# Optimization experiments

Hardware: AMD Instinct MI355X
Metric: run time of the kernel (lower is better)

Reference implementation:

```python
import jax, jax.numpy as jnp
import numpy as np

DIM = 1024
NUM_HEADS = 16
HEAD_DIM = DIM // NUM_HEADS
MLP_HIDDEN = 4 * DIM
SCALE = HEAD_DIM ** -0.5
EPS = 1e-5


def setup_inputs() -> dict:
    key = jax.random.key(0)
    ks = jax.random.split(key, 6)
    s = (2.0 / DIM) ** 0.5
    sd = (2.0 / MLP_HIDDEN) ** 0.5
    return {
        "x": jax.random.normal(ks[0], (2, 2048, DIM), dtype=jnp.float32),
        "attn_qkv_weight": jax.random.normal(ks[1], (3 * DIM, DIM), dtype=jnp.float32) * s,
        "attn_out_weight": jax.random.normal(ks[2], (DIM, DIM), dtype=jnp.float32) * s,
        "norm1_weight": jnp.ones((DIM,), jnp.float32),
        "norm1_bias": jnp.zeros((DIM,), jnp.float32),
        "mlp_gate_weight": jax.random.normal(ks[3], (MLP_HIDDEN, DIM), dtype=jnp.float32) * s,
        "mlp_up_weight": jax.random.normal(ks[4], (MLP_HIDDEN, DIM), dtype=jnp.float32) * s,
        "mlp_down_weight": jax.random.normal(ks[5], (DIM, MLP_HIDDEN), dtype=jnp.float32) * sd,
        "norm2_weight": jnp.ones((DIM,), jnp.float32),
        "norm2_bias": jnp.zeros((DIM,), jnp.float32),
    }


def _layer_norm(x, w, b):
    mean = x.mean(axis=-1, keepdims=True)
    var = jnp.mean(jnp.square(x - mean), axis=-1, keepdims=True)
    return (x - mean) / jnp.sqrt(var + EPS) * w + b


def reference(x, attn_qkv_weight, attn_out_weight, norm1_weight, norm1_bias,
              mlp_gate_weight, mlp_up_weight, mlp_down_weight, norm2_weight, norm2_bias):
    B, S, D = x.shape
    residual1 = x
    xn = _layer_norm(x, norm1_weight, norm1_bias)
    qkv = xn @ attn_qkv_weight.T                      # [B,S,3D]
    qkv = qkv.reshape(B, S, 3, NUM_HEADS, HEAD_DIM).transpose(2, 0, 3, 1, 4)
    q, k, v = qkv[0], qkv[1], qkv[2]                  # [B,H,S,hd]
    scores = jnp.einsum('bhqd,bhkd->bhqk', q, k) * SCALE  # full O(S^2) matrix
    attn = jax.nn.softmax(scores, axis=-1)            # no causal mask (default False)
    out = jnp.einsum('bhqk,bhkd->bhqd', attn, v)      # [B,H,S,hd]
    out = out.transpose(0, 2, 1, 3).reshape(B, S, D)
    x2 = residual1 + out @ attn_out_weight.T
    xn2 = _layer_norm(x2, norm2_weight, norm2_bias)
    gate = xn2 @ mlp_gate_weight.T
    up = xn2 @ mlp_up_weight.T
    hidden = jax.nn.silu(gate) * up
    return x2 + hidden @ mlp_down_weight.T
```

## Files before the change

### kernel.cpp

```cpp
#include <hip/hip_runtime.h>

typedef float f32x4 __attribute__((ext_vector_type(4)));
typedef __bf16 bf16x8 __attribute__((ext_vector_type(8)));
typedef unsigned int u32;

#define DEV __device__ __forceinline__

DEV void gload_lds16(const void* g, void* l) {
  __builtin_amdgcn_global_load_lds(
      (const __attribute__((address_space(1))) u32*)g,
      (__attribute__((address_space(3))) u32*)l, 16, 0, 0);
}

DEV int xcd_swz(int flat, int nwg) {
  return (flat & 7) * (nwg >> 3) + (flat >> 3);
}

__global__ __launch_bounds__(256) void cvt_bf16(const float* __restrict__ in,
                                                __bf16* __restrict__ o, int n) {
  int i = (blockIdx.x * 256 + threadIdx.x) * 8;
  if (i >= n) return;
  float4 a = *(const float4*)(in + i);
  float4 b = *(const float4*)(in + i + 4);
  union { bf16x8 v; __bf16 e[8]; } u;
  u.e[0] = (__bf16)a.x; u.e[1] = (__bf16)a.y; u.e[2] = (__bf16)a.z; u.e[3] = (__bf16)a.w;
  u.e[4] = (__bf16)b.x; u.e[5] = (__bf16)b.y; u.e[6] = (__bf16)b.z; u.e[7] = (__bf16)b.w;
  *(bf16x8*)(o + i) = u.v;
}

__global__ __launch_bounds__(256) void ln_kernel(const float* __restrict__ x,
                                                 const float* __restrict__ w,
                                                 const float* __restrict__ b,
                                                 __bf16* __restrict__ o) {
  const int row = blockIdx.x, tid = threadIdx.x;
  const float4 v = ((const float4*)(x + (size_t)row * 1024))[tid];
  float s  = v.x + v.y + v.z + v.w;
  float s2 = v.x * v.x + v.y * v.y + v.z * v.z + v.w * v.w;
  for (int off = 32; off; off >>= 1) {
    s  += __shfl_down(s, off);
    s2 += __shfl_down(s2, off);
  }
  __shared__ float rs[4], rs2[4];
  if ((tid & 63) == 0) { rs[tid >> 6] = s; rs2[tid >> 6] = s2; }
  __syncthreads();
  float S = rs[0] + rs[1] + rs[2] + rs[3];
  float S2 = rs2[0] + rs2[1] + rs2[2] + rs2[3];
  float mean = S * (1.0f / 1024.0f);
  float var = S2 * (1.0f / 1024.0f) - mean * mean;
  float inv = rsqrtf(var + 1e-5f);
  const float4 wv = ((const float4*)w)[tid];
  const float4 bv = ((const float4*)b)[tid];
  union { ushort4 u4; __bf16 e[4]; } u;
  u.e[0] = (__bf16)((v.x - mean) * inv * wv.x + bv.x);
  u.e[1] = (__bf16)((v.y - mean) * inv * wv.y + bv.y);
  u.e[2] = (__bf16)((v.z - mean) * inv * wv.z + bv.z);
  u.e[3] = (__bf16)((v.w - mean) * inv * wv.w + bv.w);
  *(ushort4*)(o + (size_t)row * 1024 + tid * 4) = u.u4;
}

template <int EPI, int MI>
__global__ __launch_bounds__(256) void gemm_bt(const __bf16* __restrict__ A,
                                               const __bf16* __restrict__ B,
                                               void* __restrict__ Cout,
                                               const float* __restrict__ Res,
                                               int M, int N, int K) {
  constexpr int BM = MI * 32;
  __shared__ __align__(16) __bf16 As[2][BM * 32];
  __shared__ __align__(16) __bf16 Bs[2][128 * 32];
  const int tid = threadIdx.x;
  const int lane = tid & 63;
  const int w = tid >> 6;
  const int wr = w >> 1, wc = w & 1;
  const int l15 = lane & 15, g = lane >> 4;

  const int nbx = gridDim.x;
  const int logical = xcd_swz(blockIdx.y * nbx + blockIdx.x, nbx * gridDim.y);
  const int bm = (logical / nbx) * BM, bn = (logical % nbx) * 128;

  f32x4 acc[MI][4] = {};

  auto stage = [&](int buf, int k0) {
#pragma unroll
    for (int p = 0; p < MI / 2; ++p) {
      const int ch = p * 256 + tid;
      const int row = ch >> 2, c = ch & 3;
      gload_lds16(A + (size_t)(bm + row) * K + k0 + c * 8, &As[buf][(p * 256 + w * 64) * 8]);
    }
#pragma unroll
    for (int p = 0; p < 2; ++p) {
      const int ch = p * 256 + tid;
      const int row = ch >> 2, c = ch & 3;
      gload_lds16(B + (size_t)(bn + row) * K + k0 + c * 8, &Bs[buf][(p * 256 + w * 64) * 8]);
    }
  };

  stage(0, 0);
  asm volatile("s_waitcnt vmcnt(0)" ::: "memory");
  __syncthreads();

  int cur = 0;
  for (int k0 = 0;;) {
    const int nk = k0 + 32;
    if (nk < K) stage(cur ^ 1, nk);
    bf16x8 af[MI], bfr[4];
#pragma unroll
    for (int i = 0; i < MI; ++i)
      af[i] = *(const bf16x8*)(&As[cur][(wr * (MI * 16) + i * 16 + l15) * 32 + g * 8]);
#pragma unroll
    for (int j = 0; j < 4; ++j)
      bfr[j] = *(const bf16x8*)(&Bs[cur][(wc * 64 + j * 16 + l15) * 32 + g * 8]);
#pragma unroll
    for (int i = 0; i < MI; ++i)
#pragma unroll
      for (int j = 0; j < 4; ++j)
        acc[i][j] = __builtin_amdgcn_mfma_f32_16x16x32_bf16(af[i], bfr[j], acc[i][j], 0, 0, 0);
    if (nk >= K) break;
    asm volatile("s_waitcnt vmcnt(0)" ::: "memory");
    __syncthreads();
    cur ^= 1;
    k0 = nk;
  }

  const int r0 = bm + wr * (MI * 16) + g * 4;
  const int c0 = bn + wc * 64 + l15;
#pragma unroll
  for (int i = 0; i < MI; ++i)
#pragma unroll
    for (int j = 0; j < 4; ++j)
#pragma unroll
      for (int r = 0; r < 4; ++r) {
        const size_t idx = (size_t)(r0 + i * 16 + r) * N + (c0 + j * 16);
        const float v = acc[i][j][r];
        if (EPI == 0) ((__bf16*)Cout)[idx] = (__bf16)v;
        else          ((float*)Cout)[idx] = v + Res[idx];
      }
}

__global__ __launch_bounds__(256, 2) void gemm_mlp(const __bf16* __restrict__ A,
                                                   const __bf16* __restrict__ BG,
                                                   const __bf16* __restrict__ BU,
                                                   __bf16* __restrict__ H,
                                                   int M, int N, int K) {
  __shared__ __align__(16) __bf16 As[2][128 * 32];
  __shared__ __align__(16) __bf16 Bg[2][128 * 32];
  __shared__ __align__(16) __bf16 Bu[2][128 * 32];
  const int tid = threadIdx.x;
  const int lane = tid & 63;
  const int w = tid >> 6;
  const int wr = w >> 1, wc = w & 1;
  const int l15 = lane & 15, g = lane >> 4;

  const int nbx = gridDim.x;
  const int logical = xcd_swz(blockIdx.y * nbx + blockIdx.x, nbx * gridDim.y);
  const int bm = (logical / nbx) * 128, bn = (logical % nbx) * 128;

  f32x4 accg[4][4] = {};
  f32x4 accu[4][4] = {};

  auto stage = [&](int buf, int k0) {
#pragma unroll
    for (int p = 0; p < 2; ++p) {
      const int ch = p * 256 + tid;
      const int row = ch >> 2, c = ch & 3;
      const int dst = (p * 256 + w * 64) * 8;
      gload_lds16(A + (size_t)(bm + row) * K + k0 + c * 8, &As[buf][dst]);
      gload_lds16(BG + (size_t)(bn + row) * K + k0 + c * 8, &Bg[buf][dst]);
      gload_lds16(BU + (size_t)(bn + row) * K + k0 + c * 8, &Bu[buf][dst]);
    }
  };

  stage(0, 0);
  asm volatile("s_waitcnt vmcnt(0)" ::: "memory");
  __syncthreads();

  int cur = 0;
  for (int k0 = 0;;) {
    const int nk = k0 + 32;
    if (nk < K) stage(cur ^ 1, nk);
    bf16x8 af[4], bgf[4], buf_[4];
#pragma unroll
    for (int i = 0; i < 4; ++i)
      af[i] = *(const bf16x8*)(&As[cur][(wr * 64 + i * 16 + l15) * 32 + g * 8]);
#pragma unroll
    for (int j = 0; j < 4; ++j) {
      bgf[j] = *(const bf16x8*)(&Bg[cur][(wc * 64 + j * 16 + l15) * 32 + g * 8]);
      buf_[j] = *(const bf16x8*)(&Bu[cur][(wc * 64 + j * 16 + l15) * 32 + g * 8]);
    }
#pragma unroll
    for (int i = 0; i < 4; ++i)
#pragma unroll
      for (int j = 0; j < 4; ++j) {
        accg[i][j] = __builtin_amdgcn_mfma_f32_16x16x32_bf16(af[i], bgf[j], accg[i][j], 0, 0, 0);
        accu[i][j] = __builtin_amdgcn_mfma_f32_16x16x32_bf16(af[i], buf_[j], accu[i][j], 0, 0, 0);
      }
    if (nk >= K) break;
    asm volatile("s_waitcnt vmcnt(0)" ::: "memory");
    __syncthreads();
    cur ^= 1;
    k0 = nk;
  }

  const int r0 = bm + wr * 64 + g * 4;
  const int c0 = bn + wc * 64 + l15;
#pragma unroll
  for (int i = 0; i < 4; ++i)
#pragma unroll
    for (int j = 0; j < 4; ++j)
#pragma unroll
      for (int r = 0; r < 4; ++r) {
        const float gt = accg[i][j][r];
        const float ut = accu[i][j][r];
        const float h = gt / (1.0f + __expf(-gt)) * ut;
        H[(size_t)(r0 + i * 16 + r) * N + (c0 + j * 16)] = (__bf16)h;
      }
}

__global__ __launch_bounds__(256) void transpose_v(const __bf16* __restrict__ qkv,
                                                   __bf16* __restrict__ vT) {
  const int st = blockIdx.x, bh = blockIdx.y;
  const int b = bh >> 4, h = bh & 15;
  __shared__ __bf16 tile[64][80];
  const int tid = threadIdx.x;
#pragma unroll
  for (int it = 0; it < 2; ++it) {
    const int idx = it * 256 + tid;
    const int r = idx >> 3, c0 = (idx & 7) * 8;
    bf16x8 v = *(const bf16x8*)(qkv + (size_t)(b * 2048 + st * 64 + r) * 3072 + 2048 + h * 64 + c0);
    *(bf16x8*)&tile[r][c0] = v;
  }
  __syncthreads();
#pragma unroll
  for (int it = 0; it < 2; ++it) {
    const int idx = it * 256 + tid;
    const int d = idx >> 3, s0 = (idx & 7) * 8;
    union { bf16x8 v; __bf16 e[8]; } u;
#pragma unroll
    for (int j = 0; j < 8; ++j) u.e[j] = tile[s0 + j][d];
    *(bf16x8*)(vT + (size_t)(bh * 64 + d) * 2048 + st * 64 + s0) = u.v;
  }
}

__global__ __launch_bounds__(256) void attn_kernel(const __bf16* __restrict__ qkv,
                                                   const __bf16* __restrict__ vT,
                                                   __bf16* __restrict__ outp) {
  const int logical = xcd_swz(blockIdx.y * 32 + blockIdx.x, 1024);
  const int qt = logical & 31, bh = logical >> 5;
  const int b = bh >> 4, h = bh & 15;
  const int tid = threadIdx.x, lane = tid & 63, w = tid >> 6;
  const int l15 = lane & 15, g = lane >> 4;
  const float CSC = 0.125f * 1.44269504f;

  __shared__ __align__(16) __bf16 Ks[64 * 64];
  __shared__ __align__(16) __bf16 Vs[64 * 64];
  __shared__ __align__(16) __bf16 Ps[4][16 * 80];

  const int qrow = qt * 64 + w * 16 + l15;
  const size_t qbase = (size_t)(b * 2048 + qrow) * 3072 + h * 64;
  const bf16x8 qf0 = *(const bf16x8*)(qkv + qbase + g * 8);
  const bf16x8 qf1 = *(const bf16x8*)(qkv + qbase + 32 + g * 8);

  f32x4 o_acc[4] = {};
  float l_r[4] = {0.f, 0.f, 0.f, 0.f};

  const size_t kgbase = (size_t)(b * 2048) * 3072 + 1024 + h * 64;
  const size_t vgbase = (size_t)bh * 64 * 2048;

  for (int t = 0; t < 32; ++t) {
    const int kv0 = t * 64;
#pragma unroll
    for (int p = 0; p < 2; ++p) {
      const int ch = p * 256 + w * 64 + lane;
      const int row = ch >> 3, c = ch & 7;
      const int gc = c ^ (row & 7);
      gload_lds16(qkv + kgbase + (size_t)(kv0 + row) * 3072 + gc * 8, Ks + (p * 256 + w * 64) * 8);
      gload_lds16(vT + vgbase + (size_t)row * 2048 + kv0 + gc * 8, Vs + (p * 256 + w * 64) * 8);
    }
    asm volatile("s_waitcnt vmcnt(0)" ::: "memory");
    __syncthreads();

    f32x4 sf[4];
    __builtin_amdgcn_s_setprio(1);
#pragma unroll
    for (int ni = 0; ni < 4; ++ni) {
      const int krow = ni * 16 + l15;
      const __bf16* kb = Ks + krow * 64;
      const bf16x8 kf0 = *(const bf16x8*)(kb + ((g ^ (krow & 7)) * 8));
      const bf16x8 kf1 = *(const bf16x8*)(kb + (((4 + g) ^ (krow & 7)) * 8));
      f32x4 z = {0.f, 0.f, 0.f, 0.f};
      z = __builtin_amdgcn_mfma_f32_16x16x32_bf16(qf0, kf0, z, 0, 0, 0);
      z = __builtin_amdgcn_mfma_f32_16x16x32_bf16(qf1, kf1, z, 0, 0, 0);
      sf[ni] = z;
    }
    __builtin_amdgcn_s_setprio(0);

#pragma unroll
    for (int ni = 0; ni < 4; ++ni)
#pragma unroll
      for (int r = 0; r < 4; ++r) {
        const float pv = exp2f(sf[ni][r] * CSC);
        sf[ni][r] = pv;
        l_r[r] += pv;
      }

    __bf16* pw = Ps[w];
#pragma unroll
    for (int ni = 0; ni < 4; ++ni)
#pragma unroll
      for (int r = 0; r < 4; ++r) {
        const int row = g * 4 + r;
        const int pc = (ni * 2 + (l15 >> 3)) ^ (row & 7);
        pw[row * 80 + pc * 8 + (l15 & 7)] = (__bf16)sf[ni][r];
      }
    asm volatile("" ::: "memory");
    const bf16x8 pa0 = *(const bf16x8*)(pw + l15 * 80 + ((g ^ (l15 & 7)) * 8));
    const bf16x8 pa1 = *(const bf16x8*)(pw + l15 * 80 + (((4 + g) ^ (l15 & 7)) * 8));

    __builtin_amdgcn_s_setprio(1);
#pragma unroll
    for (int ni = 0; ni < 4; ++ni) {
      const int vrow = ni * 16 + l15;
      const __bf16* vb = Vs + vrow * 64;
      const bf16x8 vf0 = *(const bf16x8*)(vb + ((g ^ (vrow & 7)) * 8));
      const bf16x8 vf1 = *(const bf16x8*)(vb + (((4 + g) ^ (vrow & 7)) * 8));
      o_acc[ni] = __builtin_amdgcn_mfma_f32_16x16x32_bf16(pa0, vf0, o_acc[ni], 0, 0, 0);
      o_acc[ni] = __builtin_amdgcn_mfma_f32_16x16x32_bf16(pa1, vf1, o_acc[ni], 0, 0, 0);
    }
    __builtin_amdgcn_s_setprio(0);
    __syncthreads();
  }

#pragma unroll
  for (int mk = 1; mk < 16; mk <<= 1)
#pragma unroll
    for (int r = 0; r < 4; ++r) l_r[r] += __shfl_xor(l_r[r], mk);
#pragma unroll
  for (int r = 0; r < 4; ++r) {
    const int orow = qt * 64 + w * 16 + g * 4 + r;
    const float invl = 1.0f / l_r[r];
#pragma unroll
    for (int ni = 0; ni < 4; ++ni)
      outp[(size_t)(b * 2048 + orow) * 1024 + h * 64 + ni * 16 + l15] =
          (__bf16)(o_acc[ni][r] * invl);
  }
}

extern "C" void kernel_launch(void* const* d_in, const int* in_sizes, int n_in,
                              void* d_out, int out_size, void* d_ws, size_t ws_size,
                              hipStream_t stream) {
  const float* x     = (const float*)d_in[0];
  const float* Wqkv  = (const float*)d_in[1];
  const float* Wout  = (const float*)d_in[2];
  const float* n1w   = (const float*)d_in[3];
  const float* n1b   = (const float*)d_in[4];
  const float* Wgate = (const float*)d_in[5];
  const float* Wup   = (const float*)d_in[6];
  const float* Wdown = (const float*)d_in[7];
  const float* n2w   = (const float*)d_in[8];
  const float* n2b   = (const float*)d_in[9];
  float* out = (float*)d_out;
  char* ws = (char*)d_ws;
  const size_t MB = 1u << 20;

  __bf16* XN  = (__bf16*)(ws + 0);
  __bf16* QKV = (__bf16*)(ws + 8 * MB);
  __bf16* VT  = (__bf16*)(ws + 32 * MB);
  __bf16* ATT = (__bf16*)(ws + 40 * MB);
  float*  X2  = (float*)(ws + 48 * MB);
  __bf16* H   = QKV;
  __bf16* WQ  = (__bf16*)(ws + 64 * MB);
  __bf16* WO  = (__bf16*)(ws + 70 * MB);
  __bf16* WG  = (__bf16*)(ws + 72 * MB);
  __bf16* WU  = (__bf16*)(ws + 80 * MB);
  __bf16* WD  = (__bf16*)(ws + 88 * MB);

  cvt_bf16<<<3145728 / 2048, 256, 0, stream>>>(Wqkv, WQ, 3145728);
  cvt_bf16<<<1048576 / 2048, 256, 0, stream>>>(Wout, WO, 1048576);
  cvt_bf16<<<4194304 / 2048, 256, 0, stream>>>(Wgate, WG, 4194304);
  cvt_bf16<<<4194304 / 2048, 256, 0, stream>>>(Wup, WU, 4194304);
  cvt_bf16<<<4194304 / 2048, 256, 0, stream>>>(Wdown, WD, 4194304);

  ln_kernel<<<4096, 256, 0, stream>>>(x, n1w, n1b, XN);
  gemm_bt<0, 4><<<dim3(24, 32), 256, 0, stream>>>(XN, WQ, QKV, nullptr, 4096, 3072, 1024);
  transpose_v<<<dim3(32, 32), 256, 0, stream>>>(QKV, VT);
  attn_kernel<<<dim3(32, 32), 256, 0, stream>>>(QKV, VT, ATT);
  gemm_bt<1, 2><<<dim3(8, 64), 256, 0, stream>>>(ATT, WO, X2, x, 4096, 1024, 1024);
  ln_kernel<<<4096, 256, 0, stream>>>(X2, n2w, n2b, XN);
  gemm_mlp<<<dim3(32, 32), 256, 0, stream>>>(XN, WG, WU, H, 4096, 4096, 1024);
  gemm_bt<1, 2><<<dim3(8, 64), 256, 0, stream>>>(H, WD, out, X2, 4096, 1024, 4096);

  (void)in_sizes; (void)n_in; (void)out_size; (void)ws_size;
}
```

Before: 355.3 us.

## Deepen GEMM prefetch with partial vmcnt waits, fragment-ordered LDS, grouped tile swizzle

Restructures the GEMM main loops so two K-tiles are in flight, waiting with partial vmcnt counts instead of draining all loads before each step. The LDS staging layout is reordered so each 16-row MFMA fragment sits contiguously, which lets each lane read with a simple lane*8 offset and avoids bank conflicts. Tile indices are also regrouped in bands of 8 row-tiles to improve L2 reuse. This adds an extra barrier per iteration and relies on hand-computed vmcnt values matching the number of loads issued per stage.

```diff
diff --git a/kernel.cpp b/kernel.cpp
--- a/kernel.cpp
+++ b/kernel.cpp
@@ -5,6 +5,7 @@
 typedef unsigned int u32;
 
 #define DEV __device__ __forceinline__
+#define WAITVM(n) asm volatile("s_waitcnt vmcnt(" #n ")" ::: "memory")
 
 DEV void gload_lds16(const void* g, void* l) {
   __builtin_amdgcn_global_load_lds(
@@ -58,6 +59,7 @@
   *(ushort4*)(o + (size_t)row * 1024 + tid * 4) = u.u4;
 }
 
+
 template <int EPI, int MI>
 __global__ __launch_bounds__(256) void gemm_bt(const __bf16* __restrict__ A,
                                                const __bf16* __restrict__ B,
@@ -65,6 +67,7 @@
                                                const float* __restrict__ Res,
                                                int M, int N, int K) {
   constexpr int BM = MI * 32;
+  constexpr int L = MI / 2 + 2;
   __shared__ __align__(16) __bf16 As[2][BM * 32];
   __shared__ __align__(16) __bf16 Bs[2][128 * 32];
   const int tid = threadIdx.x;
@@ -75,7 +78,9 @@
 
   const int nbx = gridDim.x;
   const int logical = xcd_swz(blockIdx.y * nbx + blockIdx.x, nbx * gridDim.y);
-  const int bm = (logical / nbx) * BM, bn = (logical % nbx) * 128;
+  const int per = 8 * nbx, grp = logical / per, rem = logical % per;
+  const int bm = (grp * 8 + (rem & 7)) * BM;
+  const int bn = (rem >> 3) * 128;
 
   f32x4 acc[MI][4] = {};
 
@@ -83,42 +88,45 @@
 #pragma unroll
     for (int p = 0; p < MI / 2; ++p) {
       const int ch = p * 256 + tid;
-      const int row = ch >> 2, c = ch & 3;
-      gload_lds16(A + (size_t)(bm + row) * K + k0 + c * 8, &As[buf][(p * 256 + w * 64) * 8]);
+      const int S = ch >> 6, u = ch & 63;
+      gload_lds16(A + (size_t)(bm + S * 16 + (u & 15)) * K + k0 + (u >> 4) * 8,
+                  &As[buf][(p * 256 + w * 64) * 8]);
     }
 #pragma unroll
     for (int p = 0; p < 2; ++p) {
       const int ch = p * 256 + tid;
-      const int row = ch >> 2, c = ch & 3;
-      gload_lds16(B + (size_t)(bn + row) * K + k0 + c * 8, &Bs[buf][(p * 256 + w * 64) * 8]);
+      const int S = ch >> 6, u = ch & 63;
+      gload_lds16(B + (size_t)(bn + S * 16 + (u & 15)) * K + k0 + (u >> 4) * 8,
+                  &Bs[buf][(p * 256 + w * 64) * 8]);
     }
   };
 
+  const int NT = K >> 5;
   stage(0, 0);
-  asm volatile("s_waitcnt vmcnt(0)" ::: "memory");
-  __syncthreads();
-
-  int cur = 0;
-  for (int k0 = 0;;) {
-    const int nk = k0 + 32;
-    if (nk < K) stage(cur ^ 1, nk);
+  stage(1, 32);
+
+  for (int t = 0; t < NT; ++t) {
+    if (t + 1 < NT) {
+      if (L == 3) WAITVM(3); else WAITVM(4);
+    } else {
+      WAITVM(0);
+    }
+    __syncthreads();
+    const int cur = t & 1;
     bf16x8 af[MI], bfr[4];
 #pragma unroll
     for (int i = 0; i < MI; ++i)
-      af[i] = *(const bf16x8*)(&As[cur][(wr * (MI * 16) + i * 16 + l15) * 32 + g * 8]);
+      af[i] = *(const bf16x8*)(&As[cur][(wr * MI + i) * 512 + lane * 8]);
 #pragma unroll
     for (int j = 0; j < 4; ++j)
-      bfr[j] = *(const bf16x8*)(&Bs[cur][(wc * 64 + j * 16 + l15) * 32 + g * 8]);
+      bfr[j] = *(const bf16x8*)(&Bs[cur][(wc * 4 + j) * 512 + lane * 8]);
 #pragma unroll
     for (int i = 0; i < MI; ++i)
 #pragma unroll
       for (int j = 0; j < 4; ++j)
         acc[i][j] = __builtin_amdgcn_mfma_f32_16x16x32_bf16(af[i], bfr[j], acc[i][j], 0, 0, 0);
-    if (nk >= K) break;
-    asm volatile("s_waitcnt vmcnt(0)" ::: "memory");
-    __syncthreads();
-    cur ^= 1;
-    k0 = nk;
+    __syncthreads();
+    if (t + 2 < NT) stage(cur, (t + 2) * 32);
   }
 
   const int r0 = bm + wr * (MI * 16) + g * 4;
@@ -152,7 +160,9 @@
 
   const int nbx = gridDim.x;
   const int logical = xcd_swz(blockIdx.y * nbx + blockIdx.x, nbx * gridDim.y);
-  const int bm = (logical / nbx) * 128, bn = (logical % nbx) * 128;
+  const int per = 8 * nbx, grp = logical / per, rem = logical % per;
+  const int bm = (grp * 8 + (rem & 7)) * 128;
+  const int bn = (rem >> 3) * 128;
 
   f32x4 accg[4][4] = {};
   f32x4 accu[4][4] = {};
@@ -161,30 +171,32 @@
 #pragma unroll
     for (int p = 0; p < 2; ++p) {
       const int ch = p * 256 + tid;
-      const int row = ch >> 2, c = ch & 3;
+      const int S = ch >> 6, u = ch & 63;
+      const size_t roff = (size_t)(S * 16 + (u & 15));
+      const int coff = (u >> 4) * 8;
       const int dst = (p * 256 + w * 64) * 8;
-      gload_lds16(A + (size_t)(bm + row) * K + k0 + c * 8, &As[buf][dst]);
-      gload_lds16(BG + (size_t)(bn + row) * K + k0 + c * 8, &Bg[buf][dst]);
-      gload_lds16(BU + (size_t)(bn + row) * K + k0 + c * 8, &Bu[buf][dst]);
+      gload_lds16(A + ((size_t)bm + roff) * K + k0 + coff, &As[buf][dst]);
+      gload_lds16(BG + ((size_t)bn + roff) * K + k0 + coff, &Bg[buf][dst]);
+      gload_lds16(BU + ((size_t)bn + roff) * K + k0 + coff, &Bu[buf][dst]);
     }
   };
 
+  const int NT = K >> 5;
   stage(0, 0);
-  asm volatile("s_waitcnt vmcnt(0)" ::: "memory");
-  __syncthreads();
-
-  int cur = 0;
-  for (int k0 = 0;;) {
-    const int nk = k0 + 32;
-    if (nk < K) stage(cur ^ 1, nk);
+  stage(1, 32);
+
+  for (int t = 0; t < NT; ++t) {
+    if (t + 1 < NT) { WAITVM(6); } else { WAITVM(0); }
+    __syncthreads();
+    const int cur = t & 1;
     bf16x8 af[4], bgf[4], buf_[4];
 #pragma unroll
     for (int i = 0; i < 4; ++i)
-      af[i] = *(const bf16x8*)(&As[cur][(wr * 64 + i * 16 + l15) * 32 + g * 8]);
+      af[i] = *(const bf16x8*)(&As[cur][(wr * 4 + i) * 512 + lane * 8]);
 #pragma unroll
     for (int j = 0; j < 4; ++j) {
-      bgf[j] = *(const bf16x8*)(&Bg[cur][(wc * 64 + j * 16 + l15) * 32 + g * 8]);
-      buf_[j] = *(const bf16x8*)(&Bu[cur][(wc * 64 + j * 16 + l15) * 32 + g * 8]);
+      bgf[j] = *(const bf16x8*)(&Bg[cur][(wc * 4 + j) * 512 + lane * 8]);
+      buf_[j] = *(const bf16x8*)(&Bu[cur][(wc * 4 + j) * 512 + lane * 8]);
     }
 #pragma unroll
     for (int i = 0; i < 4; ++i)
@@ -193,11 +205,8 @@
         accg[i][j] = __builtin_amdgcn_mfma_f32_16x16x32_bf16(af[i], bgf[j], accg[i][j], 0, 0, 0);
         accu[i][j] = __builtin_amdgcn_mfma_f32_16x16x32_bf16(af[i], buf_[j], accu[i][j], 0, 0, 0);
       }
-    if (nk >= K) break;
-    asm volatile("s_waitcnt vmcnt(0)" ::: "memory");
-    __syncthreads();
-    cur ^= 1;
-    k0 = nk;
+    __syncthreads();
+    if (t + 2 < NT) stage(cur, (t + 2) * 32);
   }
 
   const int r0 = bm + wr * 64 + g * 4;
```

New measurement: 383.0 us. 7.8% more time.
